# Performance work log

Hardware: AMD Instinct MI355X
Metric: run time of the kernel (lower is better)

## Reference

```python
import jax, jax.numpy as jnp
import numpy as np

B, R, L, F, H = 65536, 12, 16, 8, 64  # batch, rss_dim, n_leds, led_feat_dim, head_dim

def setup_inputs() -> dict:
    key = jax.random.key(0)
    ks = jax.random.split(key, 20)
    p = lambda k, shp, s=0.1: (jax.random.normal(k, shp, dtype=jnp.float32) * s)
    return {
        "rss_t": jax.random.uniform(ks[0], (B, R, 1), dtype=jnp.float32),
        "led_features": jax.random.normal(ks[1], (B, L, F), dtype=jnp.float32),
        "led_positions": jax.random.normal(ks[2], (B, L, 3), dtype=jnp.float32),
        "prev_pos": jax.random.normal(ks[3], (B, 3), dtype=jnp.float32),
        "freq_mask": jax.random.randint(ks[4], (R, L), 0, 2).astype(jnp.int32),
        # intensity_gate: Linear(1,16) -> ReLU -> Linear(16,1) -> Sigmoid
        "gw1": p(ks[5], (1, 16)), "gb1": p(ks[6], (16,)),
        "gw2": p(ks[7], (16, 1)), "gb2": p(ks[8], (1,)),
        # query_proj: Linear(1,32) -> ReLU -> Linear(32,64)
        "qw1": p(ks[9], (1, 32)), "qb1": p(ks[10], (32,)),
        "qw2": p(ks[11], (32, H)), "qb2": p(ks[12], (H,)),
        # key_proj: Linear(F+3,32) -> ReLU -> Linear(32,64)
        "kw1": p(ks[13], (F + 3, 32)), "kb1": p(ks[14], (32,)),
        "kw2": p(ks[15], (32, H)), "kb2": p(ks[16], (H,)),
        "sigma": jnp.float32(0.5),
    }

def reference(rss_t, led_features, led_positions, prev_pos, freq_mask,
              gw1, gb1, gw2, gb2, qw1, qb1, qw2, qb2, kw1, kb1, kw2, kb2, sigma):
    # intensity gate with hard threshold
    gate = jax.nn.sigmoid(jax.nn.relu(rss_t @ gw1 + gb1) @ gw2 + gb2)  # [B,R,1]
    iw = (rss_t > 0.5).astype(rss_t.dtype) * gate                      # [B,R,1]
    # query / key projections
    Q = jax.nn.relu((rss_t * iw) @ qw1 + qb1) @ qw2 + qb2              # [B,R,H]
    led_input = jnp.concatenate([led_features, led_positions], axis=-1)  # [B,L,F+3]
    K = jax.nn.relu(led_input @ kw1 + kb1) @ kw2 + kb2                 # [B,L,H]
    scores = jnp.einsum("brh,blh->brl", Q, K)                          # [B,R,L]
    # distance bias
    dist_sq = jnp.sum((prev_pos[:, None, :] - led_positions) ** 2, axis=-1)  # [B,L]
    scores = scores - dist_sq[:, None, :] / (2.0 * sigma ** 2)
    # mask + softmax
    neg = jnp.finfo(scores.dtype).min
    scores = jnp.where(freq_mask[None, :, :] == 0, neg, scores)
    attn = jax.nn.softmax(scores, axis=-1)                             # [B,R,L]
    return attn, iw.squeeze(-1)
```

## Files before the change

kernel.cpp:

```cpp
#include <hip/hip_runtime.h>

#define B_TOT 65536
#define R 12
#define L 16
#define F 8
#define NB 16
#define BH_LSTRIDE 36
#define BH_BSTRIDE 580
#define NEG_MIN -3.402823466e38f


__global__ __launch_bounds__(256) void nfh_precompute(
    const float* __restrict__ qw2, const float* __restrict__ qb2,
    const float* __restrict__ kw2, const float* __restrict__ kb2,
    float* __restrict__ ws)
{
    const int t = threadIdx.x;
    for (int e = t; e < 1024; e += 256) {
        const int i = e >> 5, j = e & 31;
        float acc = 0.f;
        for (int h = 0; h < 64; ++h) acc = fmaf(qw2[i * 64 + h], kw2[j * 64 + h], acc);
        ws[e] = acc;
    }
    if (t < 32) {
        float acc = 0.f;
        for (int h = 0; h < 64; ++h) acc = fmaf(qw2[t * 64 + h], kb2[h], acc);
        ws[1024 + t] = acc;
    } else if (t < 64) {
        const int j = t - 32;
        float acc = 0.f;
        for (int h = 0; h < 64; ++h) acc = fmaf(kw2[j * 64 + h], qb2[h], acc);
        ws[1056 + j] = acc;
    } else if (t == 64) {
        float acc = 0.f;
        for (int h = 0; h < 64; ++h) acc = fmaf(qb2[h], kb2[h], acc);
        ws[1088] = acc;
    }
}

__global__ __launch_bounds__(256) void nfh_main(
    const float* __restrict__ rss,
    const float* __restrict__ feat,
    const float* __restrict__ pos,
    const float* __restrict__ prev,
    const int*   __restrict__ fmask,
    const float* __restrict__ gw1, const float* __restrict__ gb1,
    const float* __restrict__ gw2, const float* __restrict__ gb2,
    const float* __restrict__ qw1, const float* __restrict__ qb1,
    const float* __restrict__ kw1, const float* __restrict__ kb1,
    const float* __restrict__ sigma_p,
    const float* __restrict__ ws,
    float* __restrict__ out)
{
    __shared__ float s_bh[NB * BH_BSTRIDE];
    __shared__ float s_vb[NB * L];

    const int t = threadIdx.x;
    const int b0 = blockIdx.x * NB;
    const float sigma = sigma_p[0];
    const float inv2s2 = 1.f / (2.f * sigma * sigma);
    const float* __restrict__ Mw = ws;
    const float* __restrict__ uw = ws + 1024;
    const float* __restrict__ vw = ws + 1056;
    const float cc = ws[1088];

    {
        const int bb = t >> 4, l = t & 15;
        const int b = b0 + bb;
        float in[11];
        const float4* f4 = (const float4*)(feat + ((size_t)b * (L * F) + l * F));
        float4 fa = f4[0], fb = f4[1];
        in[0] = fa.x; in[1] = fa.y; in[2] = fa.z; in[3] = fa.w;
        in[4] = fb.x; in[5] = fb.y; in[6] = fb.z; in[7] = fb.w;
        const float* pp = pos + ((size_t)b * (L * 3) + l * 3);
        in[8] = pp[0]; in[9] = pp[1]; in[10] = pp[2];

        float dsq = 0.f;
        #pragma unroll
        for (int m = 0; m < 3; ++m) {
            float d = prev[b * 3 + m] - in[8 + m];
            dsq = fmaf(d, d, dsq);
        }

        float bh[32];
        #pragma unroll
        for (int j = 0; j < 32; ++j) bh[j] = kb1[j];
        #pragma unroll
        for (int m = 0; m < 11; ++m) {
            const float im = in[m];
            #pragma unroll
            for (int j = 0; j < 32; ++j) bh[j] = fmaf(im, kw1[m * 32 + j], bh[j]);
        }
        float vb = 0.f;
        #pragma unroll
        for (int j = 0; j < 32; ++j) {
            bh[j] = fmaxf(bh[j], 0.f);
            vb = fmaf(vw[j], bh[j], vb);
        }
        s_vb[bb * L + l] = vb + cc - dsq * inv2s2;

        float4* dst = (float4*)&s_bh[bb * BH_BSTRIDE + l * BH_LSTRIDE];
        #pragma unroll
        for (int q = 0; q < 8; ++q)
            dst[q] = make_float4(bh[q * 4], bh[q * 4 + 1], bh[q * 4 + 2], bh[q * 4 + 3]);
    }
    __syncthreads();

    if (t < NB * R) {
        const int bb = t / R;
        const int r = t - bb * R;
        const int b = b0 + bb;

        const float x = rss[(size_t)b0 * R + t];

        float z = gb2[0];
        #pragma unroll
        for (int i = 0; i < 16; ++i) {
            float h = fmaxf(fmaf(x, gw1[i], gb1[i]), 0.f);
            z = fmaf(h, gw2[i], z);
        }
        const float gate = 1.f / (1.f + __expf(-z));
        const float iw = (x > 0.5f) ? gate : 0.f;
        out[(size_t)B_TOT * R * L + (size_t)b0 * R + t] = iw;

        const float xq = x * iw;

        float a[32];
        float d = 0.f;
        #pragma unroll
        for (int i = 0; i < 32; ++i) {
            a[i] = fmaxf(fmaf(xq, qw1[i], qb1[i]), 0.f);
            d = fmaf(a[i], uw[i], d);
        }

        float tt[32];
        #pragma unroll
        for (int j = 0; j < 32; ++j) tt[j] = 0.f;
        #pragma unroll 2
        for (int i = 0; i < 32; ++i) {
            const float ai = a[i];
            #pragma unroll
            for (int j = 0; j < 32; ++j) tt[j] = fmaf(ai, Mw[i * 32 + j], tt[j]);
        }

        float sc[16];
        const float* bhp = &s_bh[bb * BH_BSTRIDE];
        #pragma unroll
        for (int l = 0; l < L; ++l) {
            const float4* bp4 = (const float4*)&bhp[l * BH_LSTRIDE];
            float acc = d + s_vb[bb * L + l];
            #pragma unroll
            for (int q = 0; q < 8; ++q) {
                float4 v4 = bp4[q];
                acc = fmaf(tt[q * 4 + 0], v4.x, acc);
                acc = fmaf(tt[q * 4 + 1], v4.y, acc);
                acc = fmaf(tt[q * 4 + 2], v4.z, acc);
                acc = fmaf(tt[q * 4 + 3], v4.w, acc);
            }
            sc[l] = (fmask[r * L + l] == 0) ? NEG_MIN : acc;
        }

        float mx = sc[0];
        #pragma unroll
        for (int l = 1; l < L; ++l) mx = fmaxf(mx, sc[l]);
        float sum = 0.f;
        #pragma unroll
        for (int l = 0; l < L; ++l) {
            sc[l] = __expf(sc[l] - mx);
            sum += sc[l];
        }
        const float inv = 1.f / sum;

        float4* op4 = (float4*)(out + (size_t)((size_t)b * R + r) * L);
        #pragma unroll
        for (int q = 0; q < 4; ++q)
            op4[q] = make_float4(sc[q * 4] * inv, sc[q * 4 + 1] * inv,
                                 sc[q * 4 + 2] * inv, sc[q * 4 + 3] * inv);
    }
}

extern "C" void kernel_launch(void* const* d_in, const int* in_sizes, int n_in,
                              void* d_out, int out_size, void* d_ws, size_t ws_size,
                              hipStream_t stream) {
    const float* rss   = (const float*)d_in[0];
    const float* feat  = (const float*)d_in[1];
    const float* pos   = (const float*)d_in[2];
    const float* prev  = (const float*)d_in[3];
    const int*   fmask = (const int*)d_in[4];
    const float* gw1   = (const float*)d_in[5];
    const float* gb1   = (const float*)d_in[6];
    const float* gw2   = (const float*)d_in[7];
    const float* gb2   = (const float*)d_in[8];
    const float* qw1   = (const float*)d_in[9];
    const float* qb1   = (const float*)d_in[10];
    const float* qw2   = (const float*)d_in[11];
    const float* qb2   = (const float*)d_in[12];
    const float* kw1   = (const float*)d_in[13];
    const float* kb1   = (const float*)d_in[14];
    const float* kw2   = (const float*)d_in[15];
    const float* kb2   = (const float*)d_in[16];
    const float* sigma = (const float*)d_in[17];
    float* out = (float*)d_out;
    float* ws  = (float*)d_ws;

    nfh_precompute<<<1, 256, 0, stream>>>(qw2, qb2, kw2, kb2, ws);
    nfh_main<<<B_TOT / NB, 256, 0, stream>>>(
        rss, feat, pos, prev, fmask,
        gw1, gb1, gw2, gb2, qw1, qb1, kw1, kb1,
        sigma, ws, out);
}
```

Measured before the change: 185.2 us.

## Exploit piecewise-linear query ReLU to precompute per-segment score tables

Since the query MLP input is scalar, the ReLU activation pattern depends only on which breakpoint interval xq falls in, so scores become affine in xq per interval. A precompute kernel sorts the 32 breakpoints and builds per-interval A/B tables contracted with the key-weight product. The main kernel then computes, for each distinct interval used in a batch row, two dot products per LED instead of a 32x32 matvec per query. It also packs the frequency mask into bitmasks and raises the occupancy hint, at the cost of extra syncs and shared-memory bookkeeping.

```diff
diff --git a/kernel.cpp b/kernel.cpp
--- a/kernel.cpp
+++ b/kernel.cpp
@@ -3,86 +3,143 @@
 #define B_TOT 65536
 #define R 12
 #define L 16
-#define F 8
 #define NB 16
-#define BH_LSTRIDE 36
-#define BH_BSTRIDE 580
 #define NEG_MIN -3.402823466e38f
 
-
-__global__ __launch_bounds__(256) void nfh_precompute(
+#define WS_V   0
+#define WS_C   32
+#define WS_PM  40
+#define WS_BP  64
+#define WS_TAB 96
+#define TROW   72
+
+__global__ __launch_bounds__(256) void nfh_pre(
+    const float* __restrict__ qw1, const float* __restrict__ qb1,
     const float* __restrict__ qw2, const float* __restrict__ qb2,
     const float* __restrict__ kw2, const float* __restrict__ kb2,
+    const int*   __restrict__ fmask,
     float* __restrict__ ws)
 {
+    __shared__ float sM[1024];
+    __shared__ float su[32];
+    __shared__ float sw1[32], sb1[32], sbp[32];
     const int t = threadIdx.x;
+
+    if (t < 32) { sw1[t] = qw1[t]; sb1[t] = qb1[t]; }
     for (int e = t; e < 1024; e += 256) {
         const int i = e >> 5, j = e & 31;
         float acc = 0.f;
         for (int h = 0; h < 64; ++h) acc = fmaf(qw2[i * 64 + h], kw2[j * 64 + h], acc);
-        ws[e] = acc;
+        sM[e] = acc;
     }
     if (t < 32) {
-        float acc = 0.f;
-        for (int h = 0; h < 64; ++h) acc = fmaf(qw2[t * 64 + h], kb2[h], acc);
-        ws[1024 + t] = acc;
-    } else if (t < 64) {
-        const int j = t - 32;
-        float acc = 0.f;
-        for (int h = 0; h < 64; ++h) acc = fmaf(kw2[j * 64 + h], qb2[h], acc);
-        ws[1056 + j] = acc;
-    } else if (t == 64) {
+        float au = 0.f, av = 0.f;
+        for (int h = 0; h < 64; ++h) {
+            au = fmaf(qw2[t * 64 + h], kb2[h], au);
+            av = fmaf(kw2[t * 64 + h], qb2[h], av);
+        }
+        su[t] = au;
+        ws[WS_V + t] = av;
+        const float w = qw1[t];
+        sbp[t] = (w != 0.f) ? (-qb1[t] / w) : 3.0e30f;
+    }
+    if (t == 64) {
         float acc = 0.f;
         for (int h = 0; h < 64; ++h) acc = fmaf(qb2[h], kb2[h], acc);
-        ws[1088] = acc;
+        ws[WS_C] = acc;
+    }
+    if (t < 12) {
+        int pm = 0;
+        for (int l = 0; l < 16; ++l) if (fmask[t * 16 + l] != 0) pm |= (1 << l);
+        ((int*)ws)[WS_PM + t] = pm;
+    }
+    __syncthreads();
+    if (t == 0) {
+        for (int i = 1; i < 32; ++i) {
+            float key = sbp[i]; int j = i - 1;
+            while (j >= 0 && sbp[j] > key) { sbp[j + 1] = sbp[j]; --j; }
+            sbp[j + 1] = key;
+        }
+    }
+    __syncthreads();
+    if (t < 32) ws[WS_BP + t] = sbp[t];
+
+    for (int task = t; task < 33 * 32 + 33; task += 256) {
+        const int m = (task < 33 * 32) ? (task >> 5) : (task - 33 * 32);
+        const float xi = (m == 0) ? sbp[0] - 1.f
+                       : ((m == 32) ? sbp[31] + 1.f
+                                    : sbp[m - 1] + 0.5f * (sbp[m] - sbp[m - 1]));
+        if (task < 33 * 32) {
+            const int j = task & 31;
+            float A = 0.f, Bv = 0.f;
+            for (int i = 0; i < 32; ++i) {
+                if (fmaf(sw1[i], xi, sb1[i]) > 0.f) {
+                    A  = fmaf(sw1[i], sM[i * 32 + j], A);
+                    Bv = fmaf(sb1[i], sM[i * 32 + j], Bv);
+                }
+            }
+            ws[WS_TAB + m * TROW + j] = A;
+            ws[WS_TAB + m * TROW + 36 + j] = Bv;
+        } else {
+            float Au = 0.f, Bu = 0.f;
+            for (int i = 0; i < 32; ++i) {
+                if (fmaf(sw1[i], xi, sb1[i]) > 0.f) {
+                    Au = fmaf(sw1[i], su[i], Au);
+                    Bu = fmaf(sb1[i], su[i], Bu);
+                }
+            }
+            ws[WS_TAB + m * TROW + 32] = Au;
+            ws[WS_TAB + m * TROW + 36 + 32] = Bu;
+        }
     }
 }
 
-__global__ __launch_bounds__(256) void nfh_main(
+__global__ __launch_bounds__(256, 4) void nfh_main(
     const float* __restrict__ rss,
     const float* __restrict__ feat,
     const float* __restrict__ pos,
     const float* __restrict__ prev,
-    const int*   __restrict__ fmask,
     const float* __restrict__ gw1, const float* __restrict__ gb1,
     const float* __restrict__ gw2, const float* __restrict__ gb2,
-    const float* __restrict__ qw1, const float* __restrict__ qb1,
     const float* __restrict__ kw1, const float* __restrict__ kb1,
     const float* __restrict__ sigma_p,
     const float* __restrict__ ws,
     float* __restrict__ out)
 {
-    __shared__ float s_bh[NB * BH_BSTRIDE];
-    __shared__ float s_vb[NB * L];
+    __shared__ float s_dA[NB * 196];
+    __shared__ float s_dB[NB * 196];
+    __shared__ int   s_km[NB * 34];
+    __shared__ int   s_kl[NB * 12];
+    __shared__ int   s_nk[NB];
 
     const int t = threadIdx.x;
     const int b0 = blockIdx.x * NB;
     const float sigma = sigma_p[0];
     const float inv2s2 = 1.f / (2.f * sigma * sigma);
-    const float* __restrict__ Mw = ws;
-    const float* __restrict__ uw = ws + 1024;
-    const float* __restrict__ vw = ws + 1056;
-    const float cc = ws[1088];
-
+    const float* __restrict__ tab = ws + WS_TAB;
+
+    for (int e = t; e < NB * 34; e += 256) s_km[e] = -1;
+    __syncthreads();
+
+    const int bb1 = t >> 4, l1 = t & 15;
+    float bh[32];
+    float vbl;
     {
-        const int bb = t >> 4, l = t & 15;
-        const int b = b0 + bb;
+        const int b = b0 + bb1;
         float in[11];
-        const float4* f4 = (const float4*)(feat + ((size_t)b * (L * F) + l * F));
-        float4 fa = f4[0], fb = f4[1];
+        const float4* f4 = (const float4*)(feat + ((size_t)b * (L * 8) + l1 * 8));
+        const float4 fa = f4[0], fb = f4[1];
         in[0] = fa.x; in[1] = fa.y; in[2] = fa.z; in[3] = fa.w;
         in[4] = fb.x; in[5] = fb.y; in[6] = fb.z; in[7] = fb.w;
-        const float* pp = pos + ((size_t)b * (L * 3) + l * 3);
+        const float* pp = pos + ((size_t)b * (L * 3) + l1 * 3);
         in[8] = pp[0]; in[9] = pp[1]; in[10] = pp[2];
 
         float dsq = 0.f;
         #pragma unroll
         for (int m = 0; m < 3; ++m) {
-            float d = prev[b * 3 + m] - in[8 + m];
+            const float d = prev[b * 3 + m] - in[8 + m];
             dsq = fmaf(d, d, dsq);
         }
-
-        float bh[32];
         #pragma unroll
         for (int j = 0; j < 32; ++j) bh[j] = kb1[j];
         #pragma unroll
@@ -91,87 +148,105 @@
             #pragma unroll
             for (int j = 0; j < 32; ++j) bh[j] = fmaf(im, kw1[m * 32 + j], bh[j]);
         }
-        float vb = 0.f;
+        float vb = ws[WS_C];
         #pragma unroll
         for (int j = 0; j < 32; ++j) {
             bh[j] = fmaxf(bh[j], 0.f);
-            vb = fmaf(vw[j], bh[j], vb);
-        }
-        s_vb[bb * L + l] = vb + cc - dsq * inv2s2;
-
-        float4* dst = (float4*)&s_bh[bb * BH_BSTRIDE + l * BH_LSTRIDE];
-        #pragma unroll
-        for (int q = 0; q < 8; ++q)
-            dst[q] = make_float4(bh[q * 4], bh[q * 4 + 1], bh[q * 4 + 2], bh[q * 4 + 3]);
-    }
-    __syncthreads();
-
+            vb = fmaf(ws[WS_V + j], bh[j], vb);
+        }
+        vbl = vb - dsq * inv2s2;
+    }
+
+    float xq = 0.f, iw = 0.f;
+    int kk = 0, bb2 = 0;
     if (t < NB * R) {
-        const int bb = t / R;
-        const int r = t - bb * R;
-        const int b = b0 + bb;
-
+        bb2 = t / R;
         const float x = rss[(size_t)b0 * R + t];
-
         float z = gb2[0];
         #pragma unroll
         for (int i = 0; i < 16; ++i) {
-            float h = fmaxf(fmaf(x, gw1[i], gb1[i]), 0.f);
+            const float h = fmaxf(fmaf(x, gw1[i], gb1[i]), 0.f);
             z = fmaf(h, gw2[i], z);
         }
         const float gate = 1.f / (1.f + __expf(-z));
-        const float iw = (x > 0.5f) ? gate : 0.f;
+        iw = (x > 0.5f) ? gate : 0.f;
         out[(size_t)B_TOT * R * L + (size_t)b0 * R + t] = iw;
-
-        const float xq = x * iw;
-
-        float a[32];
-        float d = 0.f;
-        #pragma unroll
-        for (int i = 0; i < 32; ++i) {
-            a[i] = fmaxf(fmaf(xq, qw1[i], qb1[i]), 0.f);
-            d = fmaf(a[i], uw[i], d);
-        }
-
-        float tt[32];
-        #pragma unroll
-        for (int j = 0; j < 32; ++j) tt[j] = 0.f;
-        #pragma unroll 2
-        for (int i = 0; i < 32; ++i) {
-            const float ai = a[i];
-            #pragma unroll
-            for (int j = 0; j < 32; ++j) tt[j] = fmaf(ai, Mw[i * 32 + j], tt[j]);
-        }
-
-        float sc[16];
-        const float* bhp = &s_bh[bb * BH_BSTRIDE];
-        #pragma unroll
-        for (int l = 0; l < L; ++l) {
-            const float4* bp4 = (const float4*)&bhp[l * BH_LSTRIDE];
-            float acc = d + s_vb[bb * L + l];
+        xq = x * iw;
+        #pragma unroll
+        for (int m = 0; m < 32; ++m) kk += (xq > ws[WS_BP + m]) ? 1 : 0;
+        s_km[bb2 * 34 + kk] = 1;
+    }
+    __syncthreads();
+
+    if (t < NB) {
+        int n = 0;
+        for (int k = 0; k < 33; ++k) {
+            if (s_km[t * 34 + k] >= 0) { s_kl[t * 12 + n] = k; s_km[t * 34 + k] = n; ++n; }
+        }
+        s_nk[t] = n;
+    }
+    __syncthreads();
+
+    {
+        const int n = s_nk[bb1];
+        for (int u = 0; u < n; ++u) {
+            const int k = s_kl[bb1 * 12 + u];
+            const float* row = tab + k * TROW;
+            const float4* ra = (const float4*)row;
+            const float4* rb = (const float4*)(row + 36);
+            float dA = row[32];
+            float dB = row[68] + vbl;
             #pragma unroll
             for (int q = 0; q < 8; ++q) {
-                float4 v4 = bp4[q];
-                acc = fmaf(tt[q * 4 + 0], v4.x, acc);
-                acc = fmaf(tt[q * 4 + 1], v4.y, acc);
-                acc = fmaf(tt[q * 4 + 2], v4.z, acc);
-                acc = fmaf(tt[q * 4 + 3], v4.w, acc);
-            }
-            sc[l] = (fmask[r * L + l] == 0) ? NEG_MIN : acc;
-        }
+                const float4 a4 = ra[q];
+                dA = fmaf(a4.x, bh[q * 4 + 0], dA);
+                dA = fmaf(a4.y, bh[q * 4 + 1], dA);
+                dA = fmaf(a4.z, bh[q * 4 + 2], dA);
+                dA = fmaf(a4.w, bh[q * 4 + 3], dA);
+            }
+            #pragma unroll
+            for (int q = 0; q < 8; ++q) {
+                const float4 b4 = rb[q];
+                dB = fmaf(b4.x, bh[q * 4 + 0], dB);
+                dB = fmaf(b4.y, bh[q * 4 + 1], dB);
+                dB = fmaf(b4.z, bh[q * 4 + 2], dB);
+                dB = fmaf(b4.w, bh[q * 4 + 3], dB);
+            }
+            s_dA[bb1 * 196 + u * 16 + l1] = dA;
+            s_dB[bb1 * 196 + u * 16 + l1] = dB;
+        }
+    }
+    __syncthreads();
+
+    if (t < NB * R) {
+        const int r2 = t - bb2 * R;
+        const int u = s_km[bb2 * 34 + kk];
+        const float4* pa = (const float4*)&s_dA[bb2 * 196 + u * 16];
+        const float4* pb = (const float4*)&s_dB[bb2 * 196 + u * 16];
+        const int pm = ((const int*)ws)[WS_PM + r2];
+
+        float sc[16];
+        #pragma unroll
+        for (int q = 0; q < 4; ++q) {
+            const float4 a4 = pa[q], b4 = pb[q];
+            sc[q * 4 + 0] = fmaf(xq, a4.x, b4.x);
+            sc[q * 4 + 1] = fmaf(xq, a4.y, b4.y);
+            sc[q * 4 + 2] = fmaf(xq, a4.z, b4.z);
+            sc[q * 4 + 3] = fmaf(xq, a4.w, b4.w);
+        }
+        #pragma unroll
+        for (int l = 0; l < 16; ++l)
+            if (!((pm >> l) & 1)) sc[l] = NEG_MIN;
 
         float mx = sc[0];
         #pragma unroll
-        for (int l = 1; l < L; ++l) mx = fmaxf(mx, sc[l]);
+        for (int l = 1; l < 16; ++l) mx = fmaxf(mx, sc[l]);
         float sum = 0.f;
         #pragma unroll
-        for (int l = 0; l < L; ++l) {
-            sc[l] = __expf(sc[l] - mx);
-            sum += sc[l];
-        }
+        for (int l = 0; l < 16; ++l) { sc[l] = __expf(sc[l] - mx); sum += sc[l]; }
         const float inv = 1.f / sum;
 
-        float4* op4 = (float4*)(out + (size_t)((size_t)b * R + r) * L);
+        float4* op4 = (float4*)(out + (size_t)((size_t)(b0 + bb2) * R + r2) * L);
         #pragma unroll
         for (int q = 0; q < 4; ++q)
             op4[q] = make_float4(sc[q * 4] * inv, sc[q * 4 + 1] * inv,
@@ -203,9 +278,9 @@
     float* out = (float*)d_out;
     float* ws  = (float*)d_ws;
 
-    nfh_precompute<<<1, 256, 0, stream>>>(qw2, qb2, kw2, kb2, ws);
+    nfh_pre<<<1, 256, 0, stream>>>(qw1, qb1, qw2, qb2, kw2, kb2, fmask, ws);
     nfh_main<<<B_TOT / NB, 256, 0, stream>>>(
-        rss, feat, pos, prev, fmask,
-        gw1, gb1, gw2, gb2, qw1, qb1, kw1, kb1,
+        rss, feat, pos, prev,
+        gw1, gb1, gw2, gb2, kw1, kb1,
         sigma, ws, out);
 }
```

After: 213.0 us. 15.0% more time.
